# Kernel optimization log

Measured on AMD Instinct MI355X. Metric: run time of the kernel, lower is better.

The kernel has to match this reference:

```python
import jax, jax.numpy as jnp
import numpy as np

N = 100000      # nodes on each bipartite side
E = 1600000     # edges
D_IN = 128      # input feature dim
H, C = 2, 50    # heads, per-head out channels
B = 64          # graphs in batch
NEG_SLOPE = 0.2 # GATConv leaky_relu slope


def setup_inputs() -> dict:
    key = jax.random.key(0)
    ks = jax.random.split(key, 12)
    glorot = lambda k, shape: (jax.random.uniform(k, shape, jnp.float32, -1.0, 1.0)
                               * jnp.sqrt(6.0 / (shape[0] + shape[-1])))
    return {
        "x_s": jax.random.normal(ks[0], (N, D_IN), jnp.float32),
        "x_t": jax.random.normal(ks[1], (N, D_IN), jnp.float32),
        "edge_index": jax.random.randint(ks[2], (2, E), 0, N, jnp.int64),
        "distances": jax.random.uniform(ks[3], (E,), jnp.float32),
        "x_s_batch": jnp.sort(jax.random.randint(ks[4], (N,), 0, B, jnp.int64)),
        "x_t_batch": jnp.sort(jax.random.randint(ks[5], (N,), 0, B, jnp.int64)),
        "W_src": glorot(ks[6], (D_IN, H * C)),
        "W_dst": glorot(ks[7], (D_IN, H * C)),
        "att_src": glorot(ks[8], (H, C)),
        "att_dst": glorot(ks[9], (H, C)),
        "bias_conv": jnp.zeros((H * C,), jnp.float32),
        "fc_w": glorot(ks[10], (H * C, 1)),
        "fc_b": jnp.zeros((1,), jnp.float32),
    }


def reference(x_s, x_t, edge_index, distances, x_s_batch, x_t_batch,
              W_src, W_dst, att_src, att_dst, bias_conv, fc_w, fc_b):
    src, dst = edge_index[0], edge_index[1]
    # Bipartite GATConv (edge_attr ignored: built with edge_dim=None)
    hs = (x_s @ W_src).reshape(N, H, C)            # [N,H,C]
    ht = (x_t @ W_dst).reshape(N, H, C)
    a_src = jnp.einsum('nhc,hc->nh', hs, att_src)  # [N,H]
    a_dst = jnp.einsum('nhc,hc->nh', ht, att_dst)
    e = jax.nn.leaky_relu(a_src[src] + a_dst[dst], NEG_SLOPE)   # [E,H]
    # segment softmax over edges sharing a target node
    m = jax.ops.segment_max(e, dst, num_segments=N)             # [N,H]
    ex = jnp.exp(e - m[dst])
    denom = jax.ops.segment_sum(ex, dst, num_segments=N)
    alpha = ex / (denom[dst] + 1e-16)                           # [E,H]
    # scatter-aggregate weighted source messages
    msg = alpha[:, :, None] * hs[src]                           # [E,H,C]
    out = jax.ops.segment_sum(msg, dst, num_segments=N)         # [N,H,C]
    out = out.reshape(N, H * C) + bias_conv
    x = jax.nn.relu(out)
    # global mean pool (original uses x_s_batch)
    pooled = jax.ops.segment_sum(x, x_s_batch, num_segments=B)
    counts = jax.ops.segment_sum(jnp.ones((N,), x.dtype), x_s_batch, num_segments=B)
    pooled = pooled / jnp.maximum(counts, 1.0)[:, None]         # [B,H*C]
    y = pooled @ fc_w + fc_b                                    # [B,1]
    return y.squeeze(-1)
```

## Files before the change

### kernel.cpp

```cpp
#include <hip/hip_runtime.h>
#include <math.h>

#define D_IN 128
#define HC 100
#define PW 128
#define CAP 64
#define NEG 0.2f
#define BINSH 9
#define NBIN 196
#define BCAP 9216
#define ACH 4096
#define YSLOT 128

typedef __attribute__((ext_vector_type(8))) short short8;
typedef __attribute__((ext_vector_type(4))) float f32x4;
typedef __attribute__((ext_vector_type(2))) float f32x2;

__device__ __forceinline__ float lrelu(float x){ return x > 0.f ? x : NEG*x; }

__device__ __forceinline__ unsigned short f2bf(float f){
  union { float f; unsigned u; } v; v.f = f;
  unsigned r = v.u + 0x7fffu + ((v.u >> 16) & 1u);
  return (unsigned short)(r >> 16);
}
__device__ __forceinline__ float bflo(unsigned u){
  union { unsigned x; float f; } v; v.x = u << 16; return v.f;
}
__device__ __forceinline__ float bfhi(unsigned u){
  union { unsigned x; float f; } v; v.x = u & 0xffff0000u; return v.f;
}

__global__ __launch_bounds__(256) void k_init(const float* __restrict__ Wd,
    const float* __restrict__ attd, const float* __restrict__ Ws,
    const float* __restrict__ bias, const float* __restrict__ fcw,
    const float* __restrict__ fcb, const int* __restrict__ xsb,
    float* __restrict__ wv, float* __restrict__ bias_p, float* __restrict__ fcwp,
    unsigned short* __restrict__ Wp, float* __restrict__ invb,
    float* __restrict__ y, int N, int B){
  __shared__ int lo[257];
  int t = threadIdx.x;
  if (blockIdx.x == 0){
    int h = t >> 7, k = t & 127;
    float s = 0.f;
    #pragma unroll
    for (int c = 0; c < 50; ++c) s += Wd[k*HC + h*50 + c] * attd[h*50 + c];
    wv[t] = s;
    if (t < 128){
      bool cv = (t < 50) || (t >= 56 && t < 106);
      int c = (t < 50) ? t : t - 6;
      bias_p[t] = cv ? bias[c] : 0.f;
      fcwp[t]   = cv ? fcw[c]  : 0.f;
    }
    if (t < B) y[t] = fcb[0];
    if (t <= B && t < 257){
      int key = t, l = 0, hi = N;
      while (l < hi){ int mid = (l+hi)>>1; if (xsb[mid] < key) l = mid+1; else hi = mid; }
      lo[t] = l;
    }
    __syncthreads();
    if (t < B){
      int c = lo[t+1] - lo[t];
      invb[t] = 1.f / (float)((c > 0) ? c : 1);
    }
  } else {
    for (int idx = t; idx < 1792; idx += 256){
      int ct = idx >> 8, kk = (idx >> 6) & 3, lane = idx & 63;
      int kb = kk*32 + (lane >> 4)*8;
      int c  = ct*16 + (lane & 15);
      #pragma unroll
      for (int j = 0; j < 8; ++j){
        float v = (c < HC) ? Ws[(size_t)(kb + j)*HC + c] : 0.f;
        Wp[idx*8 + j] = f2bf(v);
      }
    }
  }
}

__global__ __launch_bounds__(256) void k_adst(const float* __restrict__ xt,
    const float* __restrict__ wv, float* __restrict__ a_dst, int N){
  __shared__ float wsh[256];
  int t = threadIdx.x;
  wsh[t] = wv[t];
  __syncthreads();
  int lane = t & 63;
  int n = blockIdx.x*4 + (t >> 6);
  if (n >= N) return;
  float2 x2 = *(const float2*)&xt[(size_t)n*D_IN + lane*2];
  float p0 = x2.x*wsh[lane*2]       + x2.y*wsh[lane*2+1];
  float p1 = x2.x*wsh[128+lane*2]   + x2.y*wsh[128+lane*2+1];
  #pragma unroll
  for (int d = 32; d >= 1; d >>= 1){ p0 += __shfl_xor(p0,d,64); p1 += __shfl_xor(p1,d,64); }
  if (lane == 0){ a_dst[n*2] = p0; a_dst[n*2+1] = p1; }
}

__global__ __launch_bounds__(256) void k_gemm(const float* __restrict__ x,
    const unsigned short* __restrict__ Wp, const float* __restrict__ att,
    unsigned short* __restrict__ hsb, float* __restrict__ a_src, int N)
{
  __shared__ unsigned short hls[64*PW];
  int t = threadIdx.x;
  int lane = t & 63, w = t >> 6;
  int qr = lane & 15, qq = lane >> 4;
  int row0 = blockIdx.x*64;

  for (int i = t; i < 4096; i += 256) ((unsigned*)hls)[i] = 0u;

  int arow = row0 + w*16 + qr;
  bool rv = arow < N;
  short8 afr[4];
  const float* xp = x + (size_t)arow*D_IN + qq*8;
  #pragma unroll
  for (int kk = 0; kk < 4; ++kk){
    float4 v0 = make_float4(0.f,0.f,0.f,0.f), v1 = v0;
    if (rv){ v0 = *(const float4*)(xp + kk*32); v1 = *(const float4*)(xp + kk*32 + 4); }
    short8 a;
    a[0]=(short)f2bf(v0.x); a[1]=(short)f2bf(v0.y); a[2]=(short)f2bf(v0.z); a[3]=(short)f2bf(v0.w);
    a[4]=(short)f2bf(v1.x); a[5]=(short)f2bf(v1.y); a[6]=(short)f2bf(v1.z); a[7]=(short)f2bf(v1.w);
    afr[kk] = a;
  }

  f32x4 acc[7];
  #pragma unroll
  for (int ct = 0; ct < 7; ++ct) acc[ct] = (f32x4){0.f,0.f,0.f,0.f};
  #pragma unroll
  for (int kk = 0; kk < 4; ++kk){
    #pragma unroll
    for (int ct = 0; ct < 7; ++ct){
      short8 b = *(const short8*)&Wp[(size_t)((ct*4+kk)*64 + lane)*8];
      acc[ct] = __builtin_amdgcn_mfma_f32_16x16x32_bf16(afr[kk], b, acc[ct], 0, 0, 0);
    }
  }

  float p0[4] = {0,0,0,0}, p1[4] = {0,0,0,0};
  #pragma unroll
  for (int ct = 0; ct < 7; ++ct){
    int c = ct*16 + qr;
    if (c < HC){
      float av = att[c];
      #pragma unroll
      for (int r = 0; r < 4; ++r){
        float v = acc[ct][r];
        if (c < 50) p0[r] += v*av; else p1[r] += v*av;
      }
    }
  }
  #pragma unroll
  for (int d = 1; d < 16; d <<= 1){
    #pragma unroll
    for (int r = 0; r < 4; ++r){
      p0[r] += __shfl_xor(p0[r], d, 64);
      p1[r] += __shfl_xor(p1[r], d, 64);
    }
  }
  if (qr == 0){
    #pragma unroll
    for (int r = 0; r < 4; ++r){
      int row = row0 + w*16 + qq*4 + r;
      if (row < N){ a_src[row*2] = p0[r]; a_src[row*2+1] = p1[r]; }
    }
  }

  __syncthreads();
  #pragma unroll
  for (int ct = 0; ct < 7; ++ct){
    int c = ct*16 + qr;
    if (c < HC){
      int p = (c < 50) ? c : c + 6;
      #pragma unroll
      for (int r = 0; r < 4; ++r)
        hls[(w*16 + qq*4 + r)*PW + p] = f2bf(acc[ct][r]);
    }
  }
  __syncthreads();
  unsigned* hg = (unsigned*)(hsb + (size_t)row0*PW);
  for (int i = t; i < 4096; i += 256) hg[i] = ((unsigned*)hls)[i];
}

__global__ __launch_bounds__(256) void k_binA(const int* __restrict__ ei,
    int* __restrict__ bincnt, int2* __restrict__ ebuf, int E)
{
  __shared__ int cnt[256], gbase[256];
  int t = threadIdx.x;
  int e0 = blockIdx.x * ACH;
  cnt[t] = 0;
  __syncthreads();

  int src[16], dst[16], rank[16];
  #pragma unroll
  for (int j = 0; j < 4; ++j){
    int e = e0 + t*16 + j*4;
    bool in = (e + 4 <= E);
    int4 s4 = in ? *(const int4*)&ei[e]     : make_int4(0,0,0,0);
    int4 d4 = in ? *(const int4*)&ei[E + e] : make_int4(-1,-1,-1,-1);
    src[j*4+0]=s4.x; src[j*4+1]=s4.y; src[j*4+2]=s4.z; src[j*4+3]=s4.w;
    dst[j*4+0]=d4.x; dst[j*4+1]=d4.y; dst[j*4+2]=d4.z; dst[j*4+3]=d4.w;
  }
  #pragma unroll
  for (int j = 0; j < 16; ++j)
    rank[j] = (dst[j] >= 0) ? atomicAdd(&cnt[dst[j] >> BINSH], 1) : -1;
  __syncthreads();
  gbase[t] = (cnt[t] > 0) ? atomicAdd(&bincnt[t], cnt[t]) : 0;
  __syncthreads();
  #pragma unroll
  for (int j = 0; j < 16; ++j){
    if (rank[j] >= 0){
      int b = dst[j] >> BINSH;
      int gp = gbase[b] + rank[j];
      if (gp < BCAP) ebuf[(size_t)b*BCAP + gp] = make_int2(src[j], dst[j]);
    }
  }
}

__global__ __launch_bounds__(1024) void k_binB(const int* __restrict__ bincnt,
    const int2* __restrict__ ebuf, int* __restrict__ cur, int* __restrict__ csrc, int N)
{
  __shared__ int cnt2[512];
  int t = threadIdx.x, b = blockIdx.x;
  if (t < 512) cnt2[t] = 0;
  __syncthreads();
  int nE = bincnt[b]; if (nE > BCAP) nE = BCAP;
  const int2* eb = ebuf + (size_t)b*BCAP;
  for (int i = t; i < nE; i += 1024){
    int2 sd = eb[i];
    int ld = sd.y & 511;
    int p = atomicAdd(&cnt2[ld], 1);
    if (p < CAP) csrc[(size_t)sd.y*CAP + p] = sd.x;
  }
  __syncthreads();
  int n = b*512 + t;
  if (t < 512 && n < N) cur[n] = cnt2[t];
}

__global__ __launch_bounds__(256) void k_agg(const int* __restrict__ cur,
    const int* __restrict__ csrc, const float* __restrict__ a_src,
    const float* __restrict__ a_dst, const unsigned short* __restrict__ hsb,
    const float* __restrict__ bias_p, const float* __restrict__ fcwp,
    const int* __restrict__ xsb, const float* __restrict__ invb,
    float* __restrict__ ypart, int N)
{
  int t = threadIdx.x;
  int lane = t & 63;
  int w = t >> 6;
  int n = blockIdx.x*4 + w;
  if (n >= N) return;

  int deg = cur[n]; if (deg > CAP) deg = CAP;
  size_t o = (size_t)n * CAP;
  float2 ad = *(const float2*)&a_dst[n*2];

  int sreg = (lane < deg) ? csrc[o + lane] : 0;

  int k = lane & 15, g = lane >> 4;
  bool actv = (k < 14);
  bool hsel = (k >= 7);

#define PREF(vv, e) { int s_ = __shfl(sreg, (e), 64); \
    vv = (actv && (e) < deg) ? *(const uint4*)&hsb[(size_t)s_*PW + k*8] \
                             : make_uint4(0u,0u,0u,0u); }

  uint4 v0, v1, v2, v3;
  PREF(v0, g) PREF(v1, 4+g) PREF(v2, 8+g) PREF(v3, 12+g)

  float e0 = -INFINITY, e1 = -INFINITY;
  if (lane < deg){
    float2 as = *(const float2*)&a_src[sreg*2];
    e0 = lrelu(as.x + ad.x);
    e1 = lrelu(as.y + ad.y);
  }
  float m0 = e0, m1 = e1;
  if (deg > 32){ m0 = fmaxf(m0, __shfl_xor(m0,32,64)); m1 = fmaxf(m1, __shfl_xor(m1,32,64)); }
  if (deg > 16){ m0 = fmaxf(m0, __shfl_xor(m0,16,64)); m1 = fmaxf(m1, __shfl_xor(m1,16,64)); }
  #pragma unroll
  for (int d = 8; d >= 1; d >>= 1){
    m0 = fmaxf(m0, __shfl_xor(m0,d,64)); m1 = fmaxf(m1, __shfl_xor(m1,d,64));
  }
  float x0 = 0.f, x1 = 0.f;
  if (lane < deg){ x0 = __expf(e0 - m0); x1 = __expf(e1 - m1); }
  float d0 = x0, d1 = x1;
  if (deg > 32){ d0 += __shfl_xor(d0,32,64); d1 += __shfl_xor(d1,32,64); }
  if (deg > 16){ d0 += __shfl_xor(d0,16,64); d1 += __shfl_xor(d1,16,64); }
  #pragma unroll
  for (int d = 8; d >= 1; d >>= 1){ d0 += __shfl_xor(d0,d,64); d1 += __shfl_xor(d1,d,64); }
  float inv0 = __builtin_amdgcn_rcpf(d0 + 1e-16f);
  float inv1 = __builtin_amdgcn_rcpf(d1 + 1e-16f);
  float al0 = x0 * inv0, al1 = x1 * inv1;

#define CONS(vv, e) { float a0_ = __shfl(al0, (e), 64); float a1_ = __shfl(al1, (e), 64); \
    float a_ = hsel ? a1_ : a0_; f32x2 av_ = {a_, a_}; \
    f32x2 h0_ = {bflo(vv.x), bfhi(vv.x)}; acc0 += av_*h0_; \
    f32x2 h1_ = {bflo(vv.y), bfhi(vv.y)}; acc1 += av_*h1_; \
    f32x2 h2_ = {bflo(vv.z), bfhi(vv.z)}; acc2 += av_*h2_; \
    f32x2 h3_ = {bflo(vv.w), bfhi(vv.w)}; acc3 += av_*h3_; }

  f32x2 acc0 = {0.f,0.f}, acc1 = {0.f,0.f}, acc2 = {0.f,0.f}, acc3 = {0.f,0.f};
  int base = 0;
  for (;;){
    CONS(v0, base+g);
    if (base + 4 >= deg) break;
    CONS(v1, base+4+g);
    if (base + 8 >= deg) break;
    CONS(v2, base+8+g);
    if (base + 12 >= deg) break;
    CONS(v3, base+12+g);
    base += 16;
    if (base >= deg) break;
    PREF(v0, base+g) PREF(v1, base+4+g) PREF(v2, base+8+g) PREF(v3, base+12+g)
  }

  float acc[8] = {acc0.x, acc0.y, acc1.x, acc1.y, acc2.x, acc2.y, acc3.x, acc3.y};
  #pragma unroll
  for (int j = 0; j < 8; ++j){
    acc[j] += __shfl_xor(acc[j], 16, 64);
    acc[j] += __shfl_xor(acc[j], 32, 64);
  }

  float s = 0.f;
  if (g == 0 && actv){
    float4 b0 = *(const float4*)&bias_p[k*8];
    float4 b1 = *(const float4*)&bias_p[k*8 + 4];
    float4 f0 = *(const float4*)&fcwp[k*8];
    float4 f1 = *(const float4*)&fcwp[k*8 + 4];
    s  = fmaxf(acc[0]+b0.x, 0.f)*f0.x + fmaxf(acc[1]+b0.y, 0.f)*f0.y
       + fmaxf(acc[2]+b0.z, 0.f)*f0.z + fmaxf(acc[3]+b0.w, 0.f)*f0.w
       + fmaxf(acc[4]+b1.x, 0.f)*f1.x + fmaxf(acc[5]+b1.y, 0.f)*f1.y
       + fmaxf(acc[6]+b1.z, 0.f)*f1.z + fmaxf(acc[7]+b1.w, 0.f)*f1.w;
  }
  #pragma unroll
  for (int d = 1; d <= 8; d <<= 1) s += __shfl_xor(s, d, 64);
  if (lane == 0){
    int b = xsb[n];
    atomicAdd(&ypart[b*YSLOT + (blockIdx.x & (YSLOT-1))], s * invb[b]);
  }
#undef PREF
#undef CONS
}

__global__ __launch_bounds__(128) void k_red(const float* __restrict__ ypart,
    float* __restrict__ y)
{
  __shared__ float ls[2];
  int b = blockIdx.x, t = threadIdx.x;
  float v = ypart[b*YSLOT + t];
  #pragma unroll
  for (int d = 32; d >= 1; d >>= 1) v += __shfl_xor(v, d, 64);
  if ((t & 63) == 0) ls[t >> 6] = v;
  __syncthreads();
  if (t == 0) y[b] += ls[0] + ls[1];
}

extern "C" void kernel_launch(void* const* d_in, const int* in_sizes, int n_in,
                              void* d_out, int out_size, void* d_ws, size_t ws_size,
                              hipStream_t stream)
{
  const float* x_s  = (const float*)d_in[0];
  const float* x_t  = (const float*)d_in[1];
  const int*   ei   = (const int*)d_in[2];
  const int*   xsb  = (const int*)d_in[4];
  const float* Ws   = (const float*)d_in[6];
  const float* Wd   = (const float*)d_in[7];
  const float* atts = (const float*)d_in[8];
  const float* attd = (const float*)d_in[9];
  const float* bias = (const float*)d_in[10];
  const float* fcw  = (const float*)d_in[11];
  const float* fcb  = (const float*)d_in[12];
  float* y = (float*)d_out;

  const int N = in_sizes[4];
  const int E = in_sizes[3];
  const int B = out_size;

  char* p = (char*)d_ws;
  auto carve = [&](size_t bytes)->char*{
    char* r = p; p += (bytes + 255) & ~(size_t)255; return r;
  };
  int*            cur    = (int*)           carve((size_t)N*4);
  int*            csrc   = (int*)           carve((size_t)N*CAP*4);
  float*          wv     = (float*)         carve(256*4);
  float*          a_src  = (float*)         carve((size_t)N*2*4);
  float*          a_dst  = (float*)         carve((size_t)N*2*4);
  unsigned short* hsb    = (unsigned short*)carve((size_t)(N+64)*PW*2);
  float*          bias_p = (float*)         carve(128*4);
  float*          fcwp   = (float*)         carve(128*4);
  unsigned short* Wp     = (unsigned short*)carve((size_t)1792*8*2);
  float*          invb   = (float*)         carve(256*4);
  int*            bincnt = (int*)           carve(256*4);
  float*          ypart  = (float*)         carve((size_t)B*YSLOT*4);
  int2*           ebuf   = (int2*)          carve((size_t)NBIN*BCAP*8);

  hipMemsetAsync(bincnt, 0, 256*4, stream);
  hipMemsetAsync(ypart, 0, (size_t)B*YSLOT*4, stream);

  k_init <<<2, 256, 0, stream>>>(Wd, attd, Ws, bias, fcw, fcb, xsb,
                                 wv, bias_p, fcwp, Wp, invb, y, N, B);
  k_adst <<<(N+3)/4, 256, 0, stream>>>(x_t, wv, a_dst, N);
  k_gemm <<<(N+63)/64, 256, 0, stream>>>(x_s, Wp, atts, hsb, a_src, N);
  k_binA <<<(E+ACH-1)/ACH, 256, 0, stream>>>(ei, bincnt, ebuf, E);
  k_binB <<<NBIN, 1024, 0, stream>>>(bincnt, ebuf, cur, csrc, N);
  k_agg  <<<(N+3)/4, 256, 0, stream>>>(cur, csrc, a_src, a_dst, hsb,
                                       bias_p, fcwp, xsb, invb, ypart, N);
  k_red  <<<B, 128, 0, stream>>>(ypart, y);
}
```

Baseline: 313.6 us.

## Fuse gemm, a_dst and binning into one launch; finer bins, padded pool slots

Merges the source GEMM, the destination attention projection and the edge-binning pass into one kernel whose blocks are split by block index, so the three independent stages run concurrently instead of as separate launches. The two memsets are replaced by zeroing inside the init kernel. Bins are halved in width (more bins, smaller capacity), which gives binB more, smaller blocks and halves its shared counter array. The pooled partial sums are spread across fewer slots, each padded to its own 128-byte line, and the per-graph 1/count scale moves into the final reduction. The risks are uneven block mixes in the fused grid and overflow of the smaller per-bin capacity.

Measured after the change: 314.2 us. No clear change (+0.2%).

```diff
diff --git a/kernel.cpp b/kernel.cpp
--- a/kernel.cpp
+++ b/kernel.cpp
@@ -6,11 +6,11 @@
 #define PW 128
 #define CAP 64
 #define NEG 0.2f
-#define BINSH 9
-#define NBIN 196
-#define BCAP 9216
+#define BINSH 8
+#define NBIN 391
+#define BCAP 4608
 #define ACH 4096
-#define YSLOT 128
+#define YSLOT 32
 
 typedef __attribute__((ext_vector_type(8))) short short8;
 typedef __attribute__((ext_vector_type(4))) float f32x4;
@@ -36,6 +36,7 @@
     const float* __restrict__ fcb, const int* __restrict__ xsb,
     float* __restrict__ wv, float* __restrict__ bias_p, float* __restrict__ fcwp,
     unsigned short* __restrict__ Wp, float* __restrict__ invb,
+    int* __restrict__ bincnt, float* __restrict__ ypart,
     float* __restrict__ y, int N, int B){
   __shared__ int lo[257];
   int t = threadIdx.x;
@@ -52,6 +53,7 @@
       fcwp[t]   = cv ? fcw[c]  : 0.f;
     }
     if (t < B) y[t] = fcb[0];
+    bincnt[t] = 0; bincnt[t + 256] = 0;
     if (t <= B && t < 257){
       int key = t, l = 0, hi = N;
       while (l < hi){ int mid = (l+hi)>>1; if (xsb[mid] < key) l = mid+1; else hi = mid; }
@@ -62,7 +64,7 @@
       int c = lo[t+1] - lo[t];
       invb[t] = 1.f / (float)((c > 0) ? c : 1);
     }
-  } else {
+  } else if (blockIdx.x == 1){
     for (int idx = t; idx < 1792; idx += 256){
       int ct = idx >> 8, kk = (idx >> 6) & 3, lane = idx & 63;
       int kb = kk*32 + (lane >> 4)*8;
@@ -73,140 +75,150 @@
         Wp[idx*8 + j] = f2bf(v);
       }
     }
-  }
-}
-
-__global__ __launch_bounds__(256) void k_adst(const float* __restrict__ xt,
-    const float* __restrict__ wv, float* __restrict__ a_dst, int N){
-  __shared__ float wsh[256];
+  } else {
+    float4 z = make_float4(0.f,0.f,0.f,0.f);
+    float4* yp4 = (float4*)ypart + (size_t)(blockIdx.x - 2)*8192;
+    for (int i = t; i < 8192; i += 256) yp4[i] = z;
+  }
+}
+
+__global__ __launch_bounds__(256) void k_fused(
+    const float* __restrict__ x_s, const unsigned short* __restrict__ Wp,
+    const float* __restrict__ atts, unsigned short* __restrict__ hsb,
+    float* __restrict__ a_src,
+    const float* __restrict__ x_t, const float* __restrict__ wv,
+    float* __restrict__ a_dst,
+    const int* __restrict__ ei, int* __restrict__ bincnt,
+    int2* __restrict__ ebuf,
+    int N, int E, int Gg, int Ga)
+{
+  __shared__ __align__(16) unsigned char smem[16384];
   int t = threadIdx.x;
-  wsh[t] = wv[t];
-  __syncthreads();
-  int lane = t & 63;
-  int n = blockIdx.x*4 + (t >> 6);
-  if (n >= N) return;
-  float2 x2 = *(const float2*)&xt[(size_t)n*D_IN + lane*2];
-  float p0 = x2.x*wsh[lane*2]       + x2.y*wsh[lane*2+1];
-  float p1 = x2.x*wsh[128+lane*2]   + x2.y*wsh[128+lane*2+1];
-  #pragma unroll
-  for (int d = 32; d >= 1; d >>= 1){ p0 += __shfl_xor(p0,d,64); p1 += __shfl_xor(p1,d,64); }
-  if (lane == 0){ a_dst[n*2] = p0; a_dst[n*2+1] = p1; }
-}
-
-__global__ __launch_bounds__(256) void k_gemm(const float* __restrict__ x,
-    const unsigned short* __restrict__ Wp, const float* __restrict__ att,
-    unsigned short* __restrict__ hsb, float* __restrict__ a_src, int N)
-{
-  __shared__ unsigned short hls[64*PW];
-  int t = threadIdx.x;
-  int lane = t & 63, w = t >> 6;
-  int qr = lane & 15, qq = lane >> 4;
-  int row0 = blockIdx.x*64;
-
-  for (int i = t; i < 4096; i += 256) ((unsigned*)hls)[i] = 0u;
-
-  int arow = row0 + w*16 + qr;
-  bool rv = arow < N;
-  short8 afr[4];
-  const float* xp = x + (size_t)arow*D_IN + qq*8;
-  #pragma unroll
-  for (int kk = 0; kk < 4; ++kk){
-    float4 v0 = make_float4(0.f,0.f,0.f,0.f), v1 = v0;
-    if (rv){ v0 = *(const float4*)(xp + kk*32); v1 = *(const float4*)(xp + kk*32 + 4); }
-    short8 a;
-    a[0]=(short)f2bf(v0.x); a[1]=(short)f2bf(v0.y); a[2]=(short)f2bf(v0.z); a[3]=(short)f2bf(v0.w);
-    a[4]=(short)f2bf(v1.x); a[5]=(short)f2bf(v1.y); a[6]=(short)f2bf(v1.z); a[7]=(short)f2bf(v1.w);
-    afr[kk] = a;
-  }
-
-  f32x4 acc[7];
-  #pragma unroll
-  for (int ct = 0; ct < 7; ++ct) acc[ct] = (f32x4){0.f,0.f,0.f,0.f};
-  #pragma unroll
-  for (int kk = 0; kk < 4; ++kk){
+  int bid = blockIdx.x;
+
+  if (bid < Gg){
+    unsigned short* hls = (unsigned short*)smem;
+    int lane = t & 63, w = t >> 6;
+    int qr = lane & 15, qq = lane >> 4;
+    int row0 = bid*64;
+
+    for (int i = t; i < 4096; i += 256) ((unsigned*)hls)[i] = 0u;
+
+    int arow = row0 + w*16 + qr;
+    bool rv = arow < N;
+    short8 afr[4];
+    const float* xp = x_s + (size_t)arow*D_IN + qq*8;
+    #pragma unroll
+    for (int kk = 0; kk < 4; ++kk){
+      float4 v0 = make_float4(0.f,0.f,0.f,0.f), v1 = v0;
+      if (rv){ v0 = *(const float4*)(xp + kk*32); v1 = *(const float4*)(xp + kk*32 + 4); }
+      short8 a;
+      a[0]=(short)f2bf(v0.x); a[1]=(short)f2bf(v0.y); a[2]=(short)f2bf(v0.z); a[3]=(short)f2bf(v0.w);
+      a[4]=(short)f2bf(v1.x); a[5]=(short)f2bf(v1.y); a[6]=(short)f2bf(v1.z); a[7]=(short)f2bf(v1.w);
+      afr[kk] = a;
+    }
+
+    f32x4 acc[7];
+    #pragma unroll
+    for (int ct = 0; ct < 7; ++ct) acc[ct] = (f32x4){0.f,0.f,0.f,0.f};
+    #pragma unroll
+    for (int kk = 0; kk < 4; ++kk){
+      #pragma unroll
+      for (int ct = 0; ct < 7; ++ct){
+        short8 b = *(const short8*)&Wp[(size_t)((ct*4+kk)*64 + lane)*8];
+        acc[ct] = __builtin_amdgcn_mfma_f32_16x16x32_bf16(afr[kk], b, acc[ct], 0, 0, 0);
+      }
+    }
+
+    float p0[4] = {0,0,0,0}, p1[4] = {0,0,0,0};
     #pragma unroll
     for (int ct = 0; ct < 7; ++ct){
-      short8 b = *(const short8*)&Wp[(size_t)((ct*4+kk)*64 + lane)*8];
-      acc[ct] = __builtin_amdgcn_mfma_f32_16x16x32_bf16(afr[kk], b, acc[ct], 0, 0, 0);
-    }
-  }
-
-  float p0[4] = {0,0,0,0}, p1[4] = {0,0,0,0};
-  #pragma unroll
-  for (int ct = 0; ct < 7; ++ct){
-    int c = ct*16 + qr;
-    if (c < HC){
-      float av = att[c];
+      int c = ct*16 + qr;
+      if (c < HC){
+        float av = atts[c];
+        #pragma unroll
+        for (int r = 0; r < 4; ++r){
+          float v = acc[ct][r];
+          if (c < 50) p0[r] += v*av; else p1[r] += v*av;
+        }
+      }
+    }
+    #pragma unroll
+    for (int d = 1; d < 16; d <<= 1){
       #pragma unroll
       for (int r = 0; r < 4; ++r){
-        float v = acc[ct][r];
-        if (c < 50) p0[r] += v*av; else p1[r] += v*av;
-      }
-    }
-  }
-  #pragma unroll
-  for (int d = 1; d < 16; d <<= 1){
-    #pragma unroll
-    for (int r = 0; r < 4; ++r){
-      p0[r] += __shfl_xor(p0[r], d, 64);
-      p1[r] += __shfl_xor(p1[r], d, 64);
-    }
-  }
-  if (qr == 0){
-    #pragma unroll
-    for (int r = 0; r < 4; ++r){
-      int row = row0 + w*16 + qq*4 + r;
-      if (row < N){ a_src[row*2] = p0[r]; a_src[row*2+1] = p1[r]; }
-    }
-  }
-
-  __syncthreads();
-  #pragma unroll
-  for (int ct = 0; ct < 7; ++ct){
-    int c = ct*16 + qr;
-    if (c < HC){
-      int p = (c < 50) ? c : c + 6;
+        p0[r] += __shfl_xor(p0[r], d, 64);
+        p1[r] += __shfl_xor(p1[r], d, 64);
+      }
+    }
+    if (qr == 0){
       #pragma unroll
-      for (int r = 0; r < 4; ++r)
-        hls[(w*16 + qq*4 + r)*PW + p] = f2bf(acc[ct][r]);
-    }
-  }
-  __syncthreads();
-  unsigned* hg = (unsigned*)(hsb + (size_t)row0*PW);
-  for (int i = t; i < 4096; i += 256) hg[i] = ((unsigned*)hls)[i];
-}
-
-__global__ __launch_bounds__(256) void k_binA(const int* __restrict__ ei,
-    int* __restrict__ bincnt, int2* __restrict__ ebuf, int E)
-{
-  __shared__ int cnt[256], gbase[256];
-  int t = threadIdx.x;
-  int e0 = blockIdx.x * ACH;
-  cnt[t] = 0;
-  __syncthreads();
-
-  int src[16], dst[16], rank[16];
-  #pragma unroll
-  for (int j = 0; j < 4; ++j){
-    int e = e0 + t*16 + j*4;
-    bool in = (e + 4 <= E);
-    int4 s4 = in ? *(const int4*)&ei[e]     : make_int4(0,0,0,0);
-    int4 d4 = in ? *(const int4*)&ei[E + e] : make_int4(-1,-1,-1,-1);
-    src[j*4+0]=s4.x; src[j*4+1]=s4.y; src[j*4+2]=s4.z; src[j*4+3]=s4.w;
-    dst[j*4+0]=d4.x; dst[j*4+1]=d4.y; dst[j*4+2]=d4.z; dst[j*4+3]=d4.w;
-  }
-  #pragma unroll
-  for (int j = 0; j < 16; ++j)
-    rank[j] = (dst[j] >= 0) ? atomicAdd(&cnt[dst[j] >> BINSH], 1) : -1;
-  __syncthreads();
-  gbase[t] = (cnt[t] > 0) ? atomicAdd(&bincnt[t], cnt[t]) : 0;
-  __syncthreads();
-  #pragma unroll
-  for (int j = 0; j < 16; ++j){
-    if (rank[j] >= 0){
-      int b = dst[j] >> BINSH;
-      int gp = gbase[b] + rank[j];
-      if (gp < BCAP) ebuf[(size_t)b*BCAP + gp] = make_int2(src[j], dst[j]);
+      for (int r = 0; r < 4; ++r){
+        int row = row0 + w*16 + qq*4 + r;
+        if (row < N){ a_src[row*2] = p0[r]; a_src[row*2+1] = p1[r]; }
+      }
+    }
+
+    __syncthreads();
+    #pragma unroll
+    for (int ct = 0; ct < 7; ++ct){
+      int c = ct*16 + qr;
+      if (c < HC){
+        int p = (c < 50) ? c : c + 6;
+        #pragma unroll
+        for (int r = 0; r < 4; ++r)
+          hls[(w*16 + qq*4 + r)*PW + p] = f2bf(acc[ct][r]);
+      }
+    }
+    __syncthreads();
+    unsigned* hg = (unsigned*)(hsb + (size_t)row0*PW);
+    for (int i = t; i < 4096; i += 256) hg[i] = ((unsigned*)hls)[i];
+
+  } else if (bid < Gg + Ga){
+    float* wsh = (float*)smem;
+    wsh[t] = wv[t];
+    __syncthreads();
+    int lane = t & 63;
+    int n = (bid - Gg)*4 + (t >> 6);
+    if (n >= N) return;
+    float2 x2 = *(const float2*)&x_t[(size_t)n*D_IN + lane*2];
+    float p0 = x2.x*wsh[lane*2]       + x2.y*wsh[lane*2+1];
+    float p1 = x2.x*wsh[128+lane*2]   + x2.y*wsh[128+lane*2+1];
+    #pragma unroll
+    for (int d = 32; d >= 1; d >>= 1){ p0 += __shfl_xor(p0,d,64); p1 += __shfl_xor(p1,d,64); }
+    if (lane == 0){ a_dst[n*2] = p0; a_dst[n*2+1] = p1; }
+
+  } else {
+    int* cnt   = (int*)smem;
+    int* gbase = (int*)smem + 512;
+    int e0 = (bid - Gg - Ga) * ACH;
+    cnt[t] = 0; cnt[t + 256] = 0;
+    __syncthreads();
+
+    int src[16], dst[16], rank[16];
+    #pragma unroll
+    for (int j = 0; j < 4; ++j){
+      int e = e0 + t*16 + j*4;
+      bool in = (e + 4 <= E);
+      int4 s4 = in ? *(const int4*)&ei[e]     : make_int4(0,0,0,0);
+      int4 d4 = in ? *(const int4*)&ei[E + e] : make_int4(-1,-1,-1,-1);
+      src[j*4+0]=s4.x; src[j*4+1]=s4.y; src[j*4+2]=s4.z; src[j*4+3]=s4.w;
+      dst[j*4+0]=d4.x; dst[j*4+1]=d4.y; dst[j*4+2]=d4.z; dst[j*4+3]=d4.w;
+    }
+    #pragma unroll
+    for (int j = 0; j < 16; ++j)
+      rank[j] = (dst[j] >= 0) ? atomicAdd(&cnt[dst[j] >> BINSH], 1) : -1;
+    __syncthreads();
+    for (int i = t; i < NBIN; i += 256)
+      gbase[i] = (cnt[i] > 0) ? atomicAdd(&bincnt[i], cnt[i]) : 0;
+    __syncthreads();
+    #pragma unroll
+    for (int j = 0; j < 16; ++j){
+      if (rank[j] >= 0){
+        int b = dst[j] >> BINSH;
+        int gp = gbase[b] + rank[j];
+        if (gp < BCAP) ebuf[(size_t)b*BCAP + gp] = make_int2(src[j], dst[j]);
+      }
     }
   }
 }
@@ -214,29 +226,28 @@
 __global__ __launch_bounds__(1024) void k_binB(const int* __restrict__ bincnt,
     const int2* __restrict__ ebuf, int* __restrict__ cur, int* __restrict__ csrc, int N)
 {
-  __shared__ int cnt2[512];
+  __shared__ int cnt2[256];
   int t = threadIdx.x, b = blockIdx.x;
-  if (t < 512) cnt2[t] = 0;
+  if (t < 256) cnt2[t] = 0;
   __syncthreads();
   int nE = bincnt[b]; if (nE > BCAP) nE = BCAP;
   const int2* eb = ebuf + (size_t)b*BCAP;
   for (int i = t; i < nE; i += 1024){
     int2 sd = eb[i];
-    int ld = sd.y & 511;
+    int ld = sd.y & 255;
     int p = atomicAdd(&cnt2[ld], 1);
     if (p < CAP) csrc[(size_t)sd.y*CAP + p] = sd.x;
   }
   __syncthreads();
-  int n = b*512 + t;
-  if (t < 512 && n < N) cur[n] = cnt2[t];
+  int n = b*256 + t;
+  if (t < 256 && n < N) cur[n] = cnt2[t];
 }
 
 __global__ __launch_bounds__(256) void k_agg(const int* __restrict__ cur,
     const int* __restrict__ csrc, const float* __restrict__ a_src,
     const float* __restrict__ a_dst, const unsigned short* __restrict__ hsb,
     const float* __restrict__ bias_p, const float* __restrict__ fcwp,
-    const int* __restrict__ xsb, const float* __restrict__ invb,
-    float* __restrict__ ypart, int N)
+    const int* __restrict__ xsb, float* __restrict__ ypart, int N)
 {
   int t = threadIdx.x;
   int lane = t & 63;
@@ -329,23 +340,20 @@
   for (int d = 1; d <= 8; d <<= 1) s += __shfl_xor(s, d, 64);
   if (lane == 0){
     int b = xsb[n];
-    atomicAdd(&ypart[b*YSLOT + (blockIdx.x & (YSLOT-1))], s * invb[b]);
+    atomicAdd(&ypart[(size_t)((b*YSLOT + (blockIdx.x & (YSLOT-1))) << 5)], s);
   }
 #undef PREF
 #undef CONS
 }
 
-__global__ __launch_bounds__(128) void k_red(const float* __restrict__ ypart,
-    float* __restrict__ y)
+__global__ __launch_bounds__(64) void k_red(const float* __restrict__ ypart,
+    const float* __restrict__ invb, float* __restrict__ y)
 {
-  __shared__ float ls[2];
   int b = blockIdx.x, t = threadIdx.x;
-  float v = ypart[b*YSLOT + t];
+  float v = (t < YSLOT) ? ypart[(size_t)((b*YSLOT + t) << 5)] : 0.f;
   #pragma unroll
-  for (int d = 32; d >= 1; d >>= 1) v += __shfl_xor(v, d, 64);
-  if ((t & 63) == 0) ls[t >> 6] = v;
-  __syncthreads();
-  if (t == 0) y[b] += ls[0] + ls[1];
+  for (int d = 16; d >= 1; d >>= 1) v += __shfl_xor(v, d, 64);
+  if (t == 0) y[b] += v * invb[b];
 }
 
 extern "C" void kernel_launch(void* const* d_in, const int* in_sizes, int n_in,
@@ -383,20 +391,21 @@
   float*          fcwp   = (float*)         carve(128*4);
   unsigned short* Wp     = (unsigned short*)carve((size_t)1792*8*2);
   float*          invb   = (float*)         carve(256*4);
-  int*            bincnt = (int*)           carve(256*4);
-  float*          ypart  = (float*)         carve((size_t)B*YSLOT*4);
+  int*            bincnt = (int*)           carve(512*4);
+  float*          ypart  = (float*)         carve((size_t)B*YSLOT*32*4);
   int2*           ebuf   = (int2*)          carve((size_t)NBIN*BCAP*8);
 
-  hipMemsetAsync(bincnt, 0, 256*4, stream);
-  hipMemsetAsync(ypart, 0, (size_t)B*YSLOT*4, stream);
-
-  k_init <<<2, 256, 0, stream>>>(Wd, attd, Ws, bias, fcw, fcb, xsb,
-                                 wv, bias_p, fcwp, Wp, invb, y, N, B);
-  k_adst <<<(N+3)/4, 256, 0, stream>>>(x_t, wv, a_dst, N);
-  k_gemm <<<(N+63)/64, 256, 0, stream>>>(x_s, Wp, atts, hsb, a_src, N);
-  k_binA <<<(E+ACH-1)/ACH, 256, 0, stream>>>(ei, bincnt, ebuf, E);
-  k_binB <<<NBIN, 1024, 0, stream>>>(bincnt, ebuf, cur, csrc, N);
-  k_agg  <<<(N+3)/4, 256, 0, stream>>>(cur, csrc, a_src, a_dst, hsb,
-                                       bias_p, fcwp, xsb, invb, ypart, N);
-  k_red  <<<B, 128, 0, stream>>>(ypart, y);
-}
+  const int Gg = (N + 63) / 64;
+  const int Ga = (N + 3) / 4;
+  const int Gb = (E + ACH - 1) / ACH;
+
+  k_init  <<<4, 256, 0, stream>>>(Wd, attd, Ws, bias, fcw, fcb, xsb,
+                                  wv, bias_p, fcwp, Wp, invb, bincnt, ypart, y, N, B);
+  k_fused <<<Gg + Ga + Gb, 256, 0, stream>>>(x_s, Wp, atts, hsb, a_src,
+                                             x_t, wv, a_dst,
+                                             ei, bincnt, ebuf, N, E, Gg, Ga);
+  k_binB  <<<NBIN, 1024, 0, stream>>>(bincnt, ebuf, cur, csrc, N);
+  k_agg   <<<(N+3)/4, 256, 0, stream>>>(cur, csrc, a_src, a_dst, hsb,
+                                        bias_p, fcwp, xsb, ypart, N);
+  k_red   <<<B, 64, 0, stream>>>(ypart, invb, y);
+}
```
